# Kernel optimization log

Hardware: AMD Instinct MI355X
Metric: run time of the kernel (lower is better)

The kernel has to match this reference:

```python
import jax, jax.numpy as jnp
import numpy as np

D_MODEL = 1024
N_HEAD = 16
D_HEAD = D_MODEL // N_HEAD
D_FF = 4096
B, S = 2, 2048
EPS = 1e-5


def setup_inputs() -> dict:
    key = jax.random.key(0)
    ks = jax.random.split(key, 16)
    sc = 1.0 / np.sqrt(D_MODEL)
    x = jax.random.normal(ks[0], (B, S, D_MODEL), dtype=jnp.float32)
    # causal mask: 1 where attention is disallowed (upper triangle)
    mask = jnp.triu(jnp.ones((S, S), dtype=jnp.int32), k=1)[None, None]
    p = {
        'x': x,
        'mask': mask,
        'wq': jax.random.normal(ks[1], (D_MODEL, D_MODEL), jnp.float32) * sc,
        'bq': jnp.zeros((D_MODEL,), jnp.float32),
        'wk': jax.random.normal(ks[2], (D_MODEL, D_MODEL), jnp.float32) * sc,
        'bk': jnp.zeros((D_MODEL,), jnp.float32),
        'wv': jax.random.normal(ks[3], (D_MODEL, D_MODEL), jnp.float32) * sc,
        'bv': jnp.zeros((D_MODEL,), jnp.float32),
        'wo': jax.random.normal(ks[4], (D_MODEL, D_MODEL), jnp.float32) * sc,
        'bo': jnp.zeros((D_MODEL,), jnp.float32),
        'w1': jax.random.normal(ks[5], (D_MODEL, D_FF), jnp.float32) * sc,
        'b1': jnp.zeros((D_FF,), jnp.float32),
        'w2': jax.random.normal(ks[6], (D_FF, D_MODEL), jnp.float32) * (1.0 / np.sqrt(D_FF)),
        'b2': jnp.zeros((D_MODEL,), jnp.float32),
        'g1': jnp.ones((D_MODEL,), jnp.float32),
        'beta1': jnp.zeros((D_MODEL,), jnp.float32),
        'g2': jnp.ones((D_MODEL,), jnp.float32),
        'beta2': jnp.zeros((D_MODEL,), jnp.float32),
    }
    return p


def _layer_norm(x, g, b):
    mu = jnp.mean(x, axis=-1, keepdims=True)
    var = jnp.mean(jnp.square(x - mu), axis=-1, keepdims=True)
    return (x - mu) * jax.lax.rsqrt(var + EPS) * g + b


def reference(x, mask, wq, bq, wk, bk, wv, bv, wo, bo, w1, b1, w2, b2, g1, beta1, g2, beta2):
    b, s, _ = x.shape
    # QKV projections -> [B, H, S, Dh]
    q = (x @ wq + bq).reshape(b, s, N_HEAD, D_HEAD).transpose(0, 2, 1, 3)
    k = (x @ wk + bk).reshape(b, s, N_HEAD, D_HEAD).transpose(0, 2, 1, 3)
    v = (x @ wv + bv).reshape(b, s, N_HEAD, D_HEAD).transpose(0, 2, 1, 3)
    scores = jnp.einsum('bhqd,bhkd->bhqk', q, k) / np.sqrt(D_HEAD)  # [B,H,S,S]
    scores = jnp.where(mask == 1, -jnp.inf, scores)
    attn = jax.nn.softmax(scores, axis=-1)
    out = jnp.einsum('bhqk,bhkd->bhqd', attn, v)
    out = out.transpose(0, 2, 1, 3).reshape(b, s, D_MODEL)
    attn_out = out @ wo + bo
    x1 = _layer_norm(x + attn_out, g1, beta1)
    ffn = jax.nn.relu(x1 @ w1 + b1) @ w2 + b2
    return _layer_norm(x1 + ffn, g2, beta2)
```

## Files before the change

kernel.cpp:

```cpp
#include <hip/hip_runtime.h>
#include <hip/hip_bf16.h>
#include <cstdint>

#define D_MODEL 1024
#define D_FF    4096
#define NHEAD   16
#define DHEAD   64
#define BATCH   2
#define SEQ     2048
#define BT      (BATCH*SEQ)
#define QKVLD   (3*D_MODEL)
#define LN_EPS  1e-5f

typedef __bf16 bf16_t;
typedef bf16_t bf16x8 __attribute__((ext_vector_type(8)));
typedef float  f32x4  __attribute__((ext_vector_type(4)));

__device__ __forceinline__ unsigned short f2b(float f){
  bf16_t h = (bf16_t)f;
  return __builtin_bit_cast(unsigned short, h);
}

__device__ __forceinline__ void gload16(const void* g, void* l){
  __builtin_amdgcn_global_load_lds(
      (const __attribute__((address_space(1))) unsigned int*)g,
      (__attribute__((address_space(3))) unsigned int*)l, 16, 0, 0);
}

__global__ __launch_bounds__(256) void cvt_f32_bf16(
    const float* __restrict__ in, unsigned short* __restrict__ out, int n){
  int i = (blockIdx.x*256 + threadIdx.x)*4;
  if (i < n){
    float4 v = *(const float4*)(in + i);
    ushort4 u; u.x=f2b(v.x); u.y=f2b(v.y); u.z=f2b(v.z); u.w=f2b(v.w);
    *(ushort4*)(out + i) = u;
  }
}

__global__ __launch_bounds__(256) void concat_bias(
    const float* __restrict__ bq, const float* __restrict__ bk,
    const float* __restrict__ bv, float* __restrict__ o){
  int i = blockIdx.x*256 + threadIdx.x;
  if (i < D_MODEL){ o[i]=bq[i]; o[D_MODEL+i]=bk[i]; o[2*D_MODEL+i]=bv[i]; }
}

__global__ __launch_bounds__(256) void transpose_cvt(
    const float* __restrict__ in, unsigned short* __restrict__ out, int R, int C){
  __shared__ float t[32][33];
  int c0 = blockIdx.x*32, r0 = blockIdx.y*32;
  int tx = threadIdx.x, ty = threadIdx.y;
  #pragma unroll
  for (int i=0;i<4;++i){ int r = ty + i*8; t[r][tx] = in[(size_t)(r0+r)*C + c0+tx]; }
  __syncthreads();
  #pragma unroll
  for (int i=0;i<4;++i){ int r = ty + i*8; out[(size_t)(c0+r)*R + r0+tx] = f2b(t[tx][r]); }
}

template<int EPI>
__global__ __launch_bounds__(512,4) void gemm128(
    const unsigned short* __restrict__ A, const unsigned short* __restrict__ Bt,
    const float* __restrict__ bias, const float* __restrict__ resid,
    float* __restrict__ outF, unsigned short* __restrict__ outB,
    int M, int N, int K){
  __shared__ __attribute__((aligned(16))) unsigned short As[2][128*64];
  __shared__ __attribute__((aligned(16))) unsigned short Bs[2][128*64];
  int tid = threadIdx.x;
  int lane = tid & 63, wave = tid >> 6;
  int lr = lane & 15, lg = lane >> 4;
  int row0 = blockIdx.x*128, col0 = blockIdx.y*128;
  int wr = (wave>>2)*64, wc = (wave&3)*32;
  int x7 = lr & 7;

  int sr = tid >> 3;
  int sl = (tid & 7) ^ (sr & 7);
  auto STAGE = [&](int k0, int buf){
    #pragma unroll
    for (int it=0; it<2; ++it){
      int c = it*512 + tid;
      int r = it*64 + sr;
      gload16(A  + (size_t)(row0+r)*K + k0 + sl*8, &As[buf][c<<3]);
      gload16(Bt + (size_t)(col0+r)*K + k0 + sl*8, &Bs[buf][c<<3]);
    }
  };

  f32x4 acc[4][2] = {};
  int nk = K >> 6;
  int t0 = 0, t1 = nk;
  if (EPI==3){ int half = nk >> 1; t0 = blockIdx.z*half; t1 = t0 + half; }
  STAGE(t0<<6, 0);
  asm volatile("s_waitcnt vmcnt(0)" ::: "memory");
  __builtin_amdgcn_s_barrier();
  int cur = 0;
  for (int t=t0; t<t1; ++t){
    if (t+1 < t1) STAGE((t+1)<<6, cur^1);
    #pragma unroll
    for (int kk=0; kk<2; ++kk){
      int sk = ((kk*4 + lg) ^ x7) << 3;
      bf16x8 af[4], bfr[2];
      #pragma unroll
      for (int mi=0;mi<4;++mi) af[mi]  = *(const bf16x8*)&As[cur][(wr+mi*16+lr)*64 + sk];
      #pragma unroll
      for (int ni=0;ni<2;++ni) bfr[ni] = *(const bf16x8*)&Bs[cur][(wc+ni*16+lr)*64 + sk];
      #pragma unroll
      for (int mi=0;mi<4;++mi)
        #pragma unroll
        for (int ni=0;ni<2;++ni)
          acc[mi][ni] = __builtin_amdgcn_mfma_f32_16x16x32_bf16(af[mi], bfr[ni], acc[mi][ni], 0,0,0);
    }
    asm volatile("s_waitcnt vmcnt(0)" ::: "memory");
    __builtin_amdgcn_s_barrier();
    cur ^= 1;
  }
  float* outP = (EPI==3) ? (outF + (size_t)blockIdx.z*((size_t)M*N)) : outF;
  #pragma unroll
  for (int mi=0;mi<4;++mi){
    int row = row0 + wr + mi*16 + (lg<<2);
    #pragma unroll
    for (int ni=0;ni<2;++ni){
      int col = col0 + wc + ni*16 + lr;
      float bs = (EPI==3) ? 0.f : bias[col];
      #pragma unroll
      for (int j=0;j<4;++j){
        size_t idx = (size_t)(row+j)*N + col;
        float v = acc[mi][ni][j] + bs;
        if (EPI==3){ outP[idx] = v; }
        else if (EPI==2){ v = fmaxf(v, 0.f); outB[idx] = f2b(v); }
        else { outB[idx] = f2b(v); }
      }
    }
  }
}

template<int EPI>
__global__ __launch_bounds__(512,2) void gemm256(
    const unsigned short* __restrict__ A, const unsigned short* __restrict__ Bt,
    const float* __restrict__ bias, unsigned short* __restrict__ outB,
    unsigned short* __restrict__ outVt,
    int M, int N, int K){
  __shared__ __attribute__((aligned(16))) unsigned short As[2][2][128*64];
  __shared__ __attribute__((aligned(16))) unsigned short Bs[2][2][128*64];
  int tid = threadIdx.x;
  int lane = tid & 63, wave = tid >> 6;
  int lr = lane & 15, lg = lane >> 4;
  int wm = wave >> 2, wn = wave & 3;
  int row0 = blockIdx.x*256, col0 = blockIdx.y*256;
  int x7 = lr & 7;
  int sr = tid >> 3;
  int sl = (tid & 7) ^ (sr & 7);

  auto STAGE_A = [&](int t, int buf, int h){
    #pragma unroll
    for (int i=0;i<2;++i){
      int c = i*512 + tid;
      int r = i*64 + sr;
      gload16(A + (size_t)(row0 + h*128 + r)*K + t*64 + sl*8, &As[buf][h][c<<3]);
    }
  };
  auto STAGE_B = [&](int t, int buf, int h){
    #pragma unroll
    for (int i=0;i<2;++i){
      int c = i*512 + tid;
      int r = i*64 + sr;
      gload16(Bt + (size_t)(col0 + h*128 + r)*K + t*64 + sl*8, &Bs[buf][h][c<<3]);
    }
  };

  f32x4 acc[8][4] = {};
  int nk = K >> 6;
  STAGE_B(0,0,0); STAGE_B(0,0,1); STAGE_A(0,0,0); STAGE_A(0,0,1);
  asm volatile("s_waitcnt vmcnt(0)" ::: "memory");
  __builtin_amdgcn_s_barrier();
  int cur = 0;
  int bq = (wn&1)*64;
  for (int t=0; t<nk; ++t){
    bool pre = (t+1 < nk);
    const unsigned short* Ah = &As[cur][wm][0];
    const unsigned short* Bh = &Bs[cur][wn>>1][0];
    bf16x8 af[4][2], bfr[4][2];
    #pragma unroll
    for (int mi=0;mi<4;++mi)
      #pragma unroll
      for (int kk=0;kk<2;++kk)
        af[mi][kk] = *(const bf16x8*)&Ah[(mi*16+lr)*64 + (((kk*4+lg)^x7)<<3)];
    #pragma unroll
    for (int ni=0;ni<2;++ni)
      #pragma unroll
      for (int kk=0;kk<2;++kk)
        bfr[ni][kk] = *(const bf16x8*)&Bh[(bq+ni*16+lr)*64 + (((kk*4+lg)^x7)<<3)];
    if (pre){ STAGE_B(t+1, cur^1, 0);
              asm volatile("s_waitcnt vmcnt(2)" ::: "memory"); }
    else    { asm volatile("s_waitcnt vmcnt(0)" ::: "memory"); }
    __builtin_amdgcn_s_barrier();
    __builtin_amdgcn_s_setprio(1);
    #pragma unroll
    for (int mi=0;mi<4;++mi)
      #pragma unroll
      for (int ni=0;ni<2;++ni)
        #pragma unroll
        for (int kk=0;kk<2;++kk)
          acc[mi][ni] = __builtin_amdgcn_mfma_f32_16x16x32_bf16(af[mi][kk], bfr[ni][kk], acc[mi][ni], 0,0,0);
    __builtin_amdgcn_s_setprio(0);
    __builtin_amdgcn_s_barrier();
    #pragma unroll
    for (int ni=2;ni<4;++ni)
      #pragma unroll
      for (int kk=0;kk<2;++kk)
        bfr[ni][kk] = *(const bf16x8*)&Bh[(bq+ni*16+lr)*64 + (((kk*4+lg)^x7)<<3)];
    if (pre) STAGE_B(t+1, cur^1, 1);
    __builtin_amdgcn_s_barrier();
    __builtin_amdgcn_s_setprio(1);
    #pragma unroll
    for (int mi=0;mi<4;++mi)
      #pragma unroll
      for (int ni=2;ni<4;++ni)
        #pragma unroll
        for (int kk=0;kk<2;++kk)
          acc[mi][ni] = __builtin_amdgcn_mfma_f32_16x16x32_bf16(af[mi][kk], bfr[ni][kk], acc[mi][ni], 0,0,0);
    __builtin_amdgcn_s_setprio(0);
    __builtin_amdgcn_s_barrier();
    #pragma unroll
    for (int mi=0;mi<4;++mi)
      #pragma unroll
      for (int kk=0;kk<2;++kk)
        af[mi][kk] = *(const bf16x8*)&Ah[((mi+4)*16+lr)*64 + (((kk*4+lg)^x7)<<3)];
    if (pre) STAGE_A(t+1, cur^1, 0);
    __builtin_amdgcn_s_barrier();
    __builtin_amdgcn_s_setprio(1);
    #pragma unroll
    for (int mi=0;mi<4;++mi)
      #pragma unroll
      for (int ni=0;ni<2;++ni)
        #pragma unroll
        for (int kk=0;kk<2;++kk)
          acc[mi+4][ni] = __builtin_amdgcn_mfma_f32_16x16x32_bf16(af[mi][kk], bfr[ni][kk], acc[mi+4][ni], 0,0,0);
    __builtin_amdgcn_s_setprio(0);
    __builtin_amdgcn_s_barrier();
    if (pre) STAGE_A(t+1, cur^1, 1);
    __builtin_amdgcn_s_barrier();
    __builtin_amdgcn_s_setprio(1);
    #pragma unroll
    for (int mi=0;mi<4;++mi)
      #pragma unroll
      for (int ni=2;ni<4;++ni)
        #pragma unroll
        for (int kk=0;kk<2;++kk)
          acc[mi+4][ni] = __builtin_amdgcn_mfma_f32_16x16x32_bf16(af[mi][kk], bfr[ni][kk], acc[mi+4][ni], 0,0,0);
    __builtin_amdgcn_s_setprio(0);
    __builtin_amdgcn_s_barrier();
    cur ^= 1;
  }
  #pragma unroll
  for (int mi=0;mi<8;++mi){
    int row = row0 + wm*128 + mi*16 + (lg<<2);
    #pragma unroll
    for (int ni=0;ni<4;++ni){
      int col = col0 + wn*64 + ni*16 + lr;
      float bs = bias[col];
      ushort4 uu;
      #pragma unroll
      for (int j=0;j<4;++j){
        size_t idx = (size_t)(row+j)*N + col;
        float v = acc[mi][ni][j] + bs;
        if (EPI==2) v = fmaxf(v, 0.f);
        unsigned short us = f2b(v);
        outB[idx] = us;
        if (j==0) uu.x=us; else if (j==1) uu.y=us; else if (j==2) uu.z=us; else uu.w=us;
      }
      if (EPI==0 && outVt && col >= 2*D_MODEL){
        int vc = col - 2*D_MODEL;
        int bh = (row>>11)*NHEAD + (vc>>6);
        int d  = vc & 63;
        int s  = row & (SEQ-1);
        *(ushort4*)&outVt[((size_t)bh*DHEAD + d)*SEQ + s] = uu;
      }
    }
  }
}

__global__ __launch_bounds__(256,2) void attn_k(
    const unsigned short* __restrict__ QKV,
    const unsigned short* __restrict__ Vt, unsigned short* __restrict__ O){
  __shared__ __attribute__((aligned(16))) unsigned short Ks[2][128*64];
  __shared__ __attribute__((aligned(16))) unsigned short Vs[2][64*128];
  __shared__ __attribute__((aligned(16))) unsigned short Ps[4][16*128];
  int tid = threadIdx.x, lane = tid&63, wave = tid>>6;
  int lr = lane&15, lg = lane>>4;
  int bid = blockIdx.x;
  int L = (bid & 7)*64 + (bid >> 3);
  int qx = L & 15;
  int bh = L >> 4;
  int b = bh>>4, h = bh&15;
  const int NT = SEQ/64;
  const float SC2 = 0.18033688011112042f;

  #pragma unroll 1
  for (int half=0; half<2; ++half){
    int qt = half ? qx : (NT-1 - qx);
    int q0w = qt*64 + wave*16;

    const unsigned short* Qrow = QKV + (size_t)(b*SEQ + q0w + lr)*QKVLD + h*DHEAD;
    bf16x8 qf[2];
    qf[0] = *(const bf16x8*)(Qrow + lg*8);
    qf[1] = *(const bf16x8*)(Qrow + 32 + lg*8);

    f32x4 oacc[4] = {};
    float m2 = -1e30f, lsum = 0.f;

    auto STAGE = [&](int t, int buf){
      int kv0 = t*128;
      #pragma unroll
      for (int it=0; it<4; ++it){
        int c = it*256 + tid;
        int rk = c>>3, slk = (c&7) ^ (rk&7);
        gload16(QKV + (size_t)(b*SEQ + kv0 + rk)*QKVLD + D_MODEL + h*DHEAD + slk*8, &Ks[buf][c<<3]);
        int rv = c>>4, slv = (c&15) ^ (rv&15);
        gload16(Vt + ((size_t)bh*DHEAD + rv)*SEQ + kv0 + slv*8, &Vs[buf][c<<3]);
      }
    };

    int nkv = (qt + 2) >> 1;
    STAGE(0, 0);
    asm volatile("s_waitcnt vmcnt(0)" ::: "memory");
    __builtin_amdgcn_s_barrier();
    int cur = 0;
    for (int t=0; t<nkv; ++t){
      if (t+1 < nkv) STAGE(t+1, cur^1);

      int kv0 = t*128;
      f32x4 sacc[8] = {};
      __builtin_amdgcn_s_setprio(1);
      #pragma unroll
      for (int kk=0;kk<2;++kk){
        #pragma unroll
        for (int ni=0;ni<8;++ni){
          int krow = ni*16 + lr;
          bf16x8 kf = *(const bf16x8*)&Ks[cur][krow*64 + (((kk*4+lg) ^ (krow&7))<<3)];
          sacc[ni] = __builtin_amdgcn_mfma_f32_16x16x32_bf16(kf, qf[kk], sacc[ni], 0,0,0);
        }
      }
      __builtin_amdgcn_s_setprio(0);
      if (t == nkv-1){
        int qpos = q0w + lr;
        #pragma unroll
        for (int ni=0;ni<8;++ni){
          f32x4 v = sacc[ni];
          #pragma unroll
          for (int j=0;j<4;++j){
            int kpos = kv0 + ni*16 + lg*4 + j;
            float sv = v[j]*SC2;
            v[j] = (kpos > qpos) ? -1e30f : sv;
          }
          sacc[ni] = v;
        }
      } else {
        #pragma unroll
        for (int ni=0;ni<8;++ni) sacc[ni] *= SC2;
      }
      f32x4 vm = sacc[0];
      #pragma unroll
      for (int ni=1;ni<8;++ni)
        #pragma unroll
        for (int j=0;j<4;++j) vm[j] = fmaxf(vm[j], sacc[ni][j]);
      float rm = fmaxf(fmaxf(vm[0],vm[1]), fmaxf(vm[2],vm[3]));
      rm = fmaxf(rm, __shfl_xor(rm, 16));
      rm = fmaxf(rm, __shfl_xor(rm, 32));
      float mnew = fmaxf(m2, rm);
      float corr = exp2f(m2 - mnew);
      m2 = mnew;
      f32x4 vs = {};
      #pragma unroll
      for (int ni=0;ni<8;++ni){
        f32x4 p;
        #pragma unroll
        for (int j=0;j<4;++j){ p[j] = exp2f(sacc[ni][j] - mnew); vs[j] += p[j]; }
        sacc[ni] = p;
      }
      float rs = (vs[0]+vs[1]) + (vs[2]+vs[3]);
      rs += __shfl_xor(rs, 16);
      rs += __shfl_xor(rs, 32);
      lsum = lsum*corr + rs;
      #pragma unroll
      for (int j=0;j<4;++j){
        float cj = __shfl(corr, lg*4 + j);
        #pragma unroll
        for (int nd=0; nd<4; ++nd) oacc[nd][j] *= cj;
      }
      #pragma unroll
      for (int ni=0;ni<8;++ni){
        ushort4 u; u.x=f2b(sacc[ni][0]); u.y=f2b(sacc[ni][1]);
                   u.z=f2b(sacc[ni][2]); u.w=f2b(sacc[ni][3]);
        int ts = ni*2 + (lg>>1);
        int a = lr*128 + (((ts ^ lr))<<3) + ((lg&1)<<2);
        *(uint2*)&Ps[wave][a] = __builtin_bit_cast(uint2, u);
      }
      __builtin_amdgcn_s_setprio(1);
      #pragma unroll
      for (int kk=0;kk<4;++kk){
        bf16x8 pa = *(const bf16x8*)&Ps[wave][lr*128 + (((kk*4+lg) ^ lr)<<3)];
        #pragma unroll
        for (int nd=0; nd<4; ++nd){
          int dr = nd*16 + lr;
          bf16x8 vf = *(const bf16x8*)&Vs[cur][dr*128 + (((kk*4+lg) ^ (dr&15))<<3)];
          oacc[nd] = __builtin_amdgcn_mfma_f32_16x16x32_bf16(pa, vf, oacc[nd], 0,0,0);
        }
      }
      __builtin_amdgcn_s_setprio(0);
      asm volatile("s_waitcnt vmcnt(0)" ::: "memory");
      __builtin_amdgcn_s_barrier();
      cur ^= 1;
    }
    #pragma unroll
    for (int j=0;j<4;++j){
      float lj = __shfl(lsum, lg*4 + j);
      float inv = 1.f / lj;
      int token = b*SEQ + q0w + lg*4 + j;
      #pragma unroll
      for (int nd=0; nd<4; ++nd)
        O[(size_t)token*D_MODEL + h*DHEAD + nd*16 + lr] = f2b(oacc[nd][j]*inv);
    }
  }
}

template<int MODE>
__global__ __launch_bounds__(256) void ln_sum_k(
    const float* __restrict__ P,
    const float* __restrict__ bias,
    const float* __restrict__ resid,
    const float* __restrict__ g, const float* __restrict__ bta,
    float* __restrict__ outF, unsigned short* __restrict__ outB){
  int row = blockIdx.x, tid = threadIdx.x;
  const size_t MN = (size_t)BT*D_MODEL;
  float4 p0 = ((const float4*)(P + (size_t)row*D_MODEL))[tid];
  float4 p1 = ((const float4*)(P + MN + (size_t)row*D_MODEL))[tid];
  float4 rr = ((const float4*)(resid + (size_t)row*D_MODEL))[tid];
  float4 bb = ((const float4*)bias)[tid];
  float4 v;
  v.x = p0.x+p1.x+bb.x+rr.x; v.y = p0.y+p1.y+bb.y+rr.y;
  v.z = p0.z+p1.z+bb.z+rr.z; v.w = p0.w+p1.w+bb.w+rr.w;
  float s = v.x+v.y+v.z+v.w;
  float q = v.x*v.x+v.y*v.y+v.z*v.z+v.w*v.w;
  #pragma unroll
  for (int d=32; d; d>>=1){ s += __shfl_xor(s, d); q += __shfl_xor(q, d); }
  __shared__ float rs[4], rq[4];
  int wave = tid>>6;
  if ((tid&63)==0){ rs[wave]=s; rq[wave]=q; }
  __syncthreads();
  s = rs[0]+rs[1]+rs[2]+rs[3];
  q = rq[0]+rq[1]+rq[2]+rq[3];
  float mu  = s * (1.f/D_MODEL);
  float var = q * (1.f/D_MODEL) - mu*mu;
  float rstd = rsqrtf(var + LN_EPS);
  float4 gg = ((const float4*)g)[tid];
  float4 be = ((const float4*)bta)[tid];
  float o0 = (v.x-mu)*rstd*gg.x + be.x;
  float o1 = (v.y-mu)*rstd*gg.y + be.y;
  float o2 = (v.z-mu)*rstd*gg.z + be.z;
  float o3 = (v.w-mu)*rstd*gg.w + be.w;
  float4 o; o.x=o0; o.y=o1; o.z=o2; o.w=o3;
  ((float4*)(outF + (size_t)row*D_MODEL))[tid] = o;
  if (MODE==0){
    ushort4 u; u.x=f2b(o0); u.y=f2b(o1); u.z=f2b(o2); u.w=f2b(o3);
    ((ushort4*)(outB + (size_t)row*D_MODEL))[tid] = u;
  }
}

extern "C" void kernel_launch(void* const* d_in, const int* in_sizes, int n_in,
                              void* d_out, int out_size, void* d_ws, size_t ws_size,
                              hipStream_t stream){
  const float* x  = (const float*)d_in[0];
  const float* wq = (const float*)d_in[2];  const float* bq = (const float*)d_in[3];
  const float* wk = (const float*)d_in[4];  const float* bk = (const float*)d_in[5];
  const float* wv = (const float*)d_in[6];  const float* bv = (const float*)d_in[7];
  const float* wo = (const float*)d_in[8];  const float* bo = (const float*)d_in[9];
  const float* w1 = (const float*)d_in[10]; const float* b1 = (const float*)d_in[11];
  const float* w2 = (const float*)d_in[12]; const float* b2 = (const float*)d_in[13];
  const float* g1 = (const float*)d_in[14]; const float* be1= (const float*)d_in[15];
  const float* g2 = (const float*)d_in[16]; const float* be2= (const float*)d_in[17];

  char* w = (char*)d_ws;
  size_t off = 0;
  auto nxt = [&](size_t bytes)->void*{
    void* p = w + off; off = (off + bytes + 255) & ~(size_t)255; return p;
  };
  unsigned short* xb    = (unsigned short*)nxt((size_t)BT*D_MODEL*2);
  unsigned short* wqkvT = (unsigned short*)nxt((size_t)QKVLD*D_MODEL*2);
  unsigned short* woT   = (unsigned short*)nxt((size_t)D_MODEL*D_MODEL*2);
  unsigned short* w1T   = (unsigned short*)nxt((size_t)D_MODEL*D_FF*2);
  unsigned short* w2T   = (unsigned short*)nxt((size_t)D_MODEL*D_FF*2);
  float*          bqkv  = (float*)nxt((size_t)QKVLD*4);
  unsigned short* QKV   = (unsigned short*)nxt((size_t)BT*QKVLD*2);
  unsigned short* VtG   = (unsigned short*)nxt((size_t)BT*D_MODEL*2);
  unsigned short* attnb = (unsigned short*)nxt((size_t)BT*D_MODEL*2);
  float*          x1f   = (float*)nxt((size_t)BT*D_MODEL*4);
  unsigned short* ffn1  = (unsigned short*)nxt((size_t)BT*D_FF*2);
  float*          Psum  = (float*)QKV;
  unsigned short* x1b   = attnb;

  dim3 tb(32,8);
  cvt_f32_bf16<<<(BT*D_MODEL)/1024, 256, 0, stream>>>(x, xb, BT*D_MODEL);
  concat_bias<<<4, 256, 0, stream>>>(bq, bk, bv, bqkv);
  transpose_cvt<<<dim3(D_MODEL/32, D_MODEL/32), tb, 0, stream>>>(wq, wqkvT,                    D_MODEL, D_MODEL);
  transpose_cvt<<<dim3(D_MODEL/32, D_MODEL/32), tb, 0, stream>>>(wk, wqkvT + D_MODEL*D_MODEL,  D_MODEL, D_MODEL);
  transpose_cvt<<<dim3(D_MODEL/32, D_MODEL/32), tb, 0, stream>>>(wv, wqkvT + 2*D_MODEL*D_MODEL,D_MODEL, D_MODEL);
  transpose_cvt<<<dim3(D_MODEL/32, D_MODEL/32), tb, 0, stream>>>(wo, woT, D_MODEL, D_MODEL);
  transpose_cvt<<<dim3(D_FF/32,    D_MODEL/32), tb, 0, stream>>>(w1, w1T, D_MODEL, D_FF);
  transpose_cvt<<<dim3(D_MODEL/32, D_FF/32),    tb, 0, stream>>>(w2, w2T, D_FF, D_MODEL);

  gemm256<0><<<dim3(BT/256, QKVLD/256), 512, 0, stream>>>(xb, wqkvT, bqkv, QKV, VtG, BT, QKVLD, D_MODEL);

  attn_k<<<512, 256, 0, stream>>>(QKV, VtG, attnb);

  gemm128<3><<<dim3(BT/128, D_MODEL/128, 2), 512, 0, stream>>>(attnb, woT, nullptr, nullptr, Psum, nullptr, BT, D_MODEL, D_MODEL);
  ln_sum_k<0><<<BT, 256, 0, stream>>>(Psum, bo, x, g1, be1, x1f, x1b);

  gemm256<2><<<dim3(BT/256, D_FF/256), 512, 0, stream>>>(x1b, w1T, b1, ffn1, nullptr, BT, D_FF, D_MODEL);

  gemm128<3><<<dim3(BT/128, D_MODEL/128, 2), 512, 0, stream>>>(ffn1, w2T, nullptr, nullptr, Psum, nullptr, BT, D_MODEL, D_FF);
  ln_sum_k<1><<<BT, 256, 0, stream>>>(Psum, b2, x1f, g2, be2, (float*)d_out, nullptr);
}
```

Measured before the change: 231.6 us.

## Store split-K partials in bf16, skip softmax rescale, merge weight transposes

The split-K output GEMMs now write their partial sums as bf16 instead of fp32, and the LayerNorm kernels read them back as bf16. This halves the traffic for the partials at some cost in precision. The attention loop skips the rescale of the running max and output accumulator when no row max grows, and the setprio hints are removed. The four square weight transposes are merged into one launch to cut launch overhead.

```diff
diff --git a/kernel.cpp b/kernel.cpp
--- a/kernel.cpp
+++ b/kernel.cpp
@@ -20,6 +20,9 @@
   bf16_t h = (bf16_t)f;
   return __builtin_bit_cast(unsigned short, h);
 }
+__device__ __forceinline__ float b2f(unsigned short u){
+  return __builtin_bit_cast(float, ((unsigned int)u)<<16);
+}
 
 __device__ __forceinline__ void gload16(const void* g, void* l){
   __builtin_amdgcn_global_load_lds(
@@ -54,6 +57,24 @@
   __syncthreads();
   #pragma unroll
   for (int i=0;i<4;++i){ int r = ty + i*8; out[(size_t)(c0+r)*R + r0+tx] = f2b(t[tx][r]); }
+}
+
+__global__ __launch_bounds__(256) void transpose_cvt4(
+    const float* __restrict__ s0, const float* __restrict__ s1,
+    const float* __restrict__ s2, const float* __restrict__ s3,
+    unsigned short* __restrict__ d0, unsigned short* __restrict__ d1,
+    unsigned short* __restrict__ d2, unsigned short* __restrict__ d3){
+  __shared__ float t[32][33];
+  int z = blockIdx.z;
+  const float* in = (z==0)?s0:(z==1)?s1:(z==2)?s2:s3;
+  unsigned short* out = (z==0)?d0:(z==1)?d1:(z==2)?d2:d3;
+  int c0 = blockIdx.x*32, r0 = blockIdx.y*32;
+  int tx = threadIdx.x, ty = threadIdx.y;
+  #pragma unroll
+  for (int i=0;i<4;++i){ int r = ty + i*8; t[r][tx] = in[(size_t)(r0+r)*D_MODEL + c0+tx]; }
+  __syncthreads();
+  #pragma unroll
+  for (int i=0;i<4;++i){ int r = ty + i*8; out[(size_t)(c0+r)*D_MODEL + r0+tx] = f2b(t[tx][r]); }
 }
 
 template<int EPI>
@@ -111,7 +132,7 @@
     __builtin_amdgcn_s_barrier();
     cur ^= 1;
   }
-  float* outP = (EPI==3) ? (outF + (size_t)blockIdx.z*((size_t)M*N)) : outF;
+  unsigned short* outBP = (EPI==3) ? (outB + (size_t)blockIdx.z*((size_t)M*N)) : outB;
   #pragma unroll
   for (int mi=0;mi<4;++mi){
     int row = row0 + wr + mi*16 + (lg<<2);
@@ -123,7 +144,7 @@
       for (int j=0;j<4;++j){
         size_t idx = (size_t)(row+j)*N + col;
         float v = acc[mi][ni][j] + bs;
-        if (EPI==3){ outP[idx] = v; }
+        if (EPI==3){ outBP[idx] = f2b(v); }
         else if (EPI==2){ v = fmaxf(v, 0.f); outB[idx] = f2b(v); }
         else { outB[idx] = f2b(v); }
       }
@@ -328,7 +349,6 @@
 
       int kv0 = t*128;
       f32x4 sacc[8] = {};
-      __builtin_amdgcn_s_setprio(1);
       #pragma unroll
       for (int kk=0;kk<2;++kk){
         #pragma unroll
@@ -338,7 +358,6 @@
           sacc[ni] = __builtin_amdgcn_mfma_f32_16x16x32_bf16(kf, qf[kk], sacc[ni], 0,0,0);
         }
       }
-      __builtin_amdgcn_s_setprio(0);
       if (t == nkv-1){
         int qpos = q0w + lr;
         #pragma unroll
@@ -364,26 +383,41 @@
       float rm = fmaxf(fmaxf(vm[0],vm[1]), fmaxf(vm[2],vm[3]));
       rm = fmaxf(rm, __shfl_xor(rm, 16));
       rm = fmaxf(rm, __shfl_xor(rm, 32));
-      float mnew = fmaxf(m2, rm);
-      float corr = exp2f(m2 - mnew);
-      m2 = mnew;
-      f32x4 vs = {};
-      #pragma unroll
-      for (int ni=0;ni<8;++ni){
-        f32x4 p;
-        #pragma unroll
-        for (int j=0;j<4;++j){ p[j] = exp2f(sacc[ni][j] - mnew); vs[j] += p[j]; }
-        sacc[ni] = p;
-      }
-      float rs = (vs[0]+vs[1]) + (vs[2]+vs[3]);
-      rs += __shfl_xor(rs, 16);
-      rs += __shfl_xor(rs, 32);
-      lsum = lsum*corr + rs;
-      #pragma unroll
-      for (int j=0;j<4;++j){
-        float cj = __shfl(corr, lg*4 + j);
-        #pragma unroll
-        for (int nd=0; nd<4; ++nd) oacc[nd][j] *= cj;
+      if (__all(rm <= m2)){
+        f32x4 vs = {};
+        #pragma unroll
+        for (int ni=0;ni<8;++ni){
+          f32x4 p;
+          #pragma unroll
+          for (int j=0;j<4;++j){ p[j] = exp2f(sacc[ni][j] - m2); vs[j] += p[j]; }
+          sacc[ni] = p;
+        }
+        float rs = (vs[0]+vs[1]) + (vs[2]+vs[3]);
+        rs += __shfl_xor(rs, 16);
+        rs += __shfl_xor(rs, 32);
+        lsum += rs;
+      } else {
+        float mnew = fmaxf(m2, rm);
+        float corr = exp2f(m2 - mnew);
+        m2 = mnew;
+        f32x4 vs = {};
+        #pragma unroll
+        for (int ni=0;ni<8;++ni){
+          f32x4 p;
+          #pragma unroll
+          for (int j=0;j<4;++j){ p[j] = exp2f(sacc[ni][j] - mnew); vs[j] += p[j]; }
+          sacc[ni] = p;
+        }
+        float rs = (vs[0]+vs[1]) + (vs[2]+vs[3]);
+        rs += __shfl_xor(rs, 16);
+        rs += __shfl_xor(rs, 32);
+        lsum = lsum*corr + rs;
+        #pragma unroll
+        for (int j=0;j<4;++j){
+          float cj = __shfl(corr, lg*4 + j);
+          #pragma unroll
+          for (int nd=0; nd<4; ++nd) oacc[nd][j] *= cj;
+        }
       }
       #pragma unroll
       for (int ni=0;ni<8;++ni){
@@ -393,7 +427,6 @@
         int a = lr*128 + (((ts ^ lr))<<3) + ((lg&1)<<2);
         *(uint2*)&Ps[wave][a] = __builtin_bit_cast(uint2, u);
       }
-      __builtin_amdgcn_s_setprio(1);
       #pragma unroll
       for (int kk=0;kk<4;++kk){
         bf16x8 pa = *(const bf16x8*)&Ps[wave][lr*128 + (((kk*4+lg) ^ lr)<<3)];
@@ -404,7 +437,6 @@
           oacc[nd] = __builtin_amdgcn_mfma_f32_16x16x32_bf16(pa, vf, oacc[nd], 0,0,0);
         }
       }
-      __builtin_amdgcn_s_setprio(0);
       asm volatile("s_waitcnt vmcnt(0)" ::: "memory");
       __builtin_amdgcn_s_barrier();
       cur ^= 1;
@@ -423,20 +455,20 @@
 
 template<int MODE>
 __global__ __launch_bounds__(256) void ln_sum_k(
-    const float* __restrict__ P,
+    const unsigned short* __restrict__ P,
     const float* __restrict__ bias,
     const float* __restrict__ resid,
     const float* __restrict__ g, const float* __restrict__ bta,
     float* __restrict__ outF, unsigned short* __restrict__ outB){
   int row = blockIdx.x, tid = threadIdx.x;
   const size_t MN = (size_t)BT*D_MODEL;
-  float4 p0 = ((const float4*)(P + (size_t)row*D_MODEL))[tid];
-  float4 p1 = ((const float4*)(P + MN + (size_t)row*D_MODEL))[tid];
+  ushort4 a0 = ((const ushort4*)(P + (size_t)row*D_MODEL))[tid];
+  ushort4 a1 = ((const ushort4*)(P + MN + (size_t)row*D_MODEL))[tid];
   float4 rr = ((const float4*)(resid + (size_t)row*D_MODEL))[tid];
   float4 bb = ((const float4*)bias)[tid];
   float4 v;
-  v.x = p0.x+p1.x+bb.x+rr.x; v.y = p0.y+p1.y+bb.y+rr.y;
-  v.z = p0.z+p1.z+bb.z+rr.z; v.w = p0.w+p1.w+bb.w+rr.w;
+  v.x = b2f(a0.x)+b2f(a1.x)+bb.x+rr.x; v.y = b2f(a0.y)+b2f(a1.y)+bb.y+rr.y;
+  v.z = b2f(a0.z)+b2f(a1.z)+bb.z+rr.z; v.w = b2f(a0.w)+b2f(a1.w)+bb.w+rr.w;
   float s = v.x+v.y+v.z+v.w;
   float q = v.x*v.x+v.y*v.y+v.z*v.z+v.w*v.w;
   #pragma unroll
@@ -493,16 +525,15 @@
   unsigned short* attnb = (unsigned short*)nxt((size_t)BT*D_MODEL*2);
   float*          x1f   = (float*)nxt((size_t)BT*D_MODEL*4);
   unsigned short* ffn1  = (unsigned short*)nxt((size_t)BT*D_FF*2);
-  float*          Psum  = (float*)QKV;
+  unsigned short* Psum  = QKV;
   unsigned short* x1b   = attnb;
 
   dim3 tb(32,8);
   cvt_f32_bf16<<<(BT*D_MODEL)/1024, 256, 0, stream>>>(x, xb, BT*D_MODEL);
   concat_bias<<<4, 256, 0, stream>>>(bq, bk, bv, bqkv);
-  transpose_cvt<<<dim3(D_MODEL/32, D_MODEL/32), tb, 0, stream>>>(wq, wqkvT,                    D_MODEL, D_MODEL);
-  transpose_cvt<<<dim3(D_MODEL/32, D_MODEL/32), tb, 0, stream>>>(wk, wqkvT + D_MODEL*D_MODEL,  D_MODEL, D_MODEL);
-  transpose_cvt<<<dim3(D_MODEL/32, D_MODEL/32), tb, 0, stream>>>(wv, wqkvT + 2*D_MODEL*D_MODEL,D_MODEL, D_MODEL);
-  transpose_cvt<<<dim3(D_MODEL/32, D_MODEL/32), tb, 0, stream>>>(wo, woT, D_MODEL, D_MODEL);
+  transpose_cvt4<<<dim3(D_MODEL/32, D_MODEL/32, 4), tb, 0, stream>>>(
+      wq, wk, wv, wo,
+      wqkvT, wqkvT + D_MODEL*D_MODEL, wqkvT + 2*D_MODEL*D_MODEL, woT);
   transpose_cvt<<<dim3(D_FF/32,    D_MODEL/32), tb, 0, stream>>>(w1, w1T, D_MODEL, D_FF);
   transpose_cvt<<<dim3(D_MODEL/32, D_FF/32),    tb, 0, stream>>>(w2, w2T, D_FF, D_MODEL);
 
@@ -510,11 +541,11 @@
 
   attn_k<<<512, 256, 0, stream>>>(QKV, VtG, attnb);
 
-  gemm128<3><<<dim3(BT/128, D_MODEL/128, 2), 512, 0, stream>>>(attnb, woT, nullptr, nullptr, Psum, nullptr, BT, D_MODEL, D_MODEL);
+  gemm128<3><<<dim3(BT/128, D_MODEL/128, 2), 512, 0, stream>>>(attnb, woT, nullptr, nullptr, nullptr, Psum, BT, D_MODEL, D_MODEL);
   ln_sum_k<0><<<BT, 256, 0, stream>>>(Psum, bo, x, g1, be1, x1f, x1b);
 
   gemm256<2><<<dim3(BT/256, D_FF/256), 512, 0, stream>>>(x1b, w1T, b1, ffn1, nullptr, BT, D_FF, D_MODEL);
 
-  gemm128<3><<<dim3(BT/128, D_MODEL/128, 2), 512, 0, stream>>>(ffn1, w2T, nullptr, nullptr, Psum, nullptr, BT, D_MODEL, D_FF);
+  gemm128<3><<<dim3(BT/128, D_MODEL/128, 2), 512, 0, stream>>>(ffn1, w2T, nullptr, nullptr, nullptr, Psum, BT, D_MODEL, D_FF);
   ln_sum_k<1><<<BT, 256, 0, stream>>>(Psum, b2, x1f, g2, be2, (float*)d_out, nullptr);
 }
```

Result: faster. 222.3 us (median of 2 runs) (-4.0%).
